# Kernel optimization log

Measured on AMD Instinct MI355X. Metric: run time of the kernel, lower is better.

## Reference

```python
import jax, jax.numpy as jnp
import numpy as np

N_NODES = 50000
N_EDGES = 800000


def setup_inputs() -> dict:
    key = jax.random.key(0)
    ks = jax.random.split(key, 9)
    d, h, hd = 128, 4, 32
    s = 1.0 / np.sqrt(d)
    return {
        "x": jax.random.normal(ks[0], (N_NODES, d), jnp.float32),
        "edge_index": jax.random.randint(ks[1], (2, N_EDGES), 0, N_NODES, jnp.int32),
        "W0": jax.random.normal(ks[2], (d, d), jnp.float32) * s,
        "att_l0": jax.random.normal(ks[3], (h, hd), jnp.float32) * s,
        "att_r0": jax.random.normal(ks[4], (h, hd), jnp.float32) * s,
        "b0": jnp.zeros((d,), jnp.float32),
        "W1": jax.random.normal(ks[5], (d, d), jnp.float32) * s,
        "att_l1": jax.random.normal(ks[6], (h, hd), jnp.float32) * s,
        "att_r1": jax.random.normal(ks[7], (h, hd), jnp.float32) * s,
        "b1": jnp.zeros((hd,), jnp.float32),
    }


def _gat_layer(x, src, dst, W, att_l, att_r, bias, concat):
    # x: [N, F_in]; W: [H*D, F_in] (torch Linear layout); att_*: [H, D]
    n = x.shape[0]
    h, d = att_l.shape
    hx = (x @ W.T).reshape(n, h, d)                     # [N,H,D]
    al = jnp.einsum('nhd,hd->nh', hx, att_l)            # [N,H]
    ar = jnp.einsum('nhd,hd->nh', hx, att_r)
    att = al[src] + ar[dst]                             # [E,H]
    att = jax.nn.leaky_relu(att, negative_slope=0.2)
    # segment softmax over destination nodes
    m = jax.ops.segment_max(att, dst, num_segments=n)   # [N,H]
    att = jnp.exp(att - m[dst])
    ssum = jax.ops.segment_sum(att, dst, num_segments=n)
    att = att / (ssum[dst] + 1e-9)                      # [E,H]
    msgs = att[:, :, None] * hx[src]                    # [E,H,D]
    out = jax.ops.segment_sum(msgs, dst, num_segments=n)  # [N,H,D]
    if concat:
        out = out.reshape(n, h * d)
    else:
        out = out.mean(axis=1)
    return out + bias


def reference(x, edge_index, W0, att_l0, att_r0, b0, W1, att_l1, att_r1, b1):
    src, dst = edge_index[0], edge_index[1]
    x = _gat_layer(x, src, dst, W0, att_l0, att_r0, b0, concat=True)
    x = jax.nn.relu(x)  # dropout is identity in eval mode
    x = _gat_layer(x, src, dst, W1, att_l1, att_r1, b1, concat=False)
    return x
```

## Files before the change

kernel.cpp:

```cpp
#include <hip/hip_runtime.h>
#include <hip/hip_bf16.h>

#define H 4
#define D 32
#define F 128
#define MAXDEG 64
#define PF 16
#define NBUCK 256
#define BUCKW 196
#define NABLK 128
#define SEGCAP 64
#define GB    1563
#define HXP   136

typedef __attribute__((ext_vector_type(8))) short bf16x8;
typedef __attribute__((ext_vector_type(4))) float f32x4;

__device__ __forceinline__ short f2bf(float v) {
    __hip_bfloat16 h = __float2bfloat16(v);
    return *reinterpret_cast<short*>(&h);
}
__device__ __forceinline__ float bf2f(short s) {
    __hip_bfloat16 h = *reinterpret_cast<__hip_bfloat16*>(&s);
    return __bfloat162float(h);
}

__device__ __forceinline__
void wconv_part(int part8, const float* __restrict__ W0, short* __restrict__ W0hi,
                short* __restrict__ W0lo, const float* __restrict__ W1,
                short* __restrict__ W1hi, short* __restrict__ W1lo) {
    const int tid = threadIdx.x;
    const float* W  = (part8 < 4) ? W0 : W1;
    short* Whi = (part8 < 4) ? W0hi : W1hi;
    short* Wlo = (part8 < 4) ? W0lo : W1lo;
    const int part = part8 & 3;
    const int base = part * (F * F / 4);
    for (int i = base + tid * 4; i < base + F * F / 4; i += 1024) {
        float4 v = *reinterpret_cast<const float4*>(W + i);
        float vv[4] = {v.x, v.y, v.z, v.w};
        short hs[4], ls[4];
#pragma unroll
        for (int j = 0; j < 4; ++j) {
            hs[j] = f2bf(vv[j]);
            ls[j] = f2bf(vv[j] - bf2f(hs[j]));
        }
        *reinterpret_cast<short4*>(Whi + i) = make_short4(hs[0], hs[1], hs[2], hs[3]);
        *reinterpret_cast<short4*>(Wlo + i) = make_short4(ls[0], ls[1], ls[2], ls[3]);
    }
}

__device__ __forceinline__
void bucketA_body(int abid, const int* __restrict__ ei, int E,
                  int* __restrict__ cntmat, unsigned int* __restrict__ buf) {
    __shared__ int lcnt[NBUCK];
    const int tid = threadIdx.x;
    lcnt[tid] = 0;
    __syncthreads();
    const int per = ((E / NABLK) + 3) & ~3;
    const int e0 = abid * per;
    const int e1 = min(e0 + per, E);
    for (int e = e0 + 4 * tid; e < e1; e += 1024) {
        int4 dv = *reinterpret_cast<const int4*>(ei + E + e);
        atomicAdd(&lcnt[dv.x / BUCKW], 1);
        atomicAdd(&lcnt[dv.y / BUCKW], 1);
        atomicAdd(&lcnt[dv.z / BUCKW], 1);
        atomicAdd(&lcnt[dv.w / BUCKW], 1);
    }
    __syncthreads();
    cntmat[abid * NBUCK + tid] = min(lcnt[tid], SEGCAP);
    lcnt[tid] = 0;
    __syncthreads();
    for (int e = e0 + 4 * tid; e < e1; e += 1024) {
        int4 sv = *reinterpret_cast<const int4*>(ei + e);
        int4 dv = *reinterpret_cast<const int4*>(ei + E + e);
        int ss[4] = {sv.x, sv.y, sv.z, sv.w};
        int dd[4] = {dv.x, dv.y, dv.z, dv.w};
#pragma unroll
        for (int j = 0; j < 4; ++j) {
            int b = dd[j] / BUCKW;
            int pos = atomicAdd(&lcnt[b], 1);
            if (pos < SEGCAP)
                buf[((size_t)b * NABLK + abid) * SEGCAP + pos] =
                    (unsigned)ss[j] | ((unsigned)(dd[j] - b * BUCKW) << 16);
        }
    }
}

__global__ __launch_bounds__(256)
void k_init(const int* __restrict__ ei, int E, int* __restrict__ cntmat,
            unsigned int* __restrict__ buf,
            const float* __restrict__ W0, short* __restrict__ W0hi,
            short* __restrict__ W0lo, const float* __restrict__ W1,
            short* __restrict__ W1hi, short* __restrict__ W1lo) {
    const int bid = blockIdx.x;
    if (bid < NABLK)
        bucketA_body(bid, ei, E, cntmat, buf);
    else
        wconv_part(bid - NABLK, W0, W0hi, W0lo, W1, W1hi, W1lo);
}

__device__ __forceinline__
void bucketB_body(int b, const unsigned int* __restrict__ buf,
                  const int* __restrict__ cntmat, int* __restrict__ deg,
                  unsigned short* __restrict__ ssrc2u, int N,
                  int* cnt, int* scnt, unsigned short* slots) {
    const int tid = threadIdx.x;
    if (tid < BUCKW) cnt[tid] = 0;
    if (tid < NABLK) scnt[tid] = cntmat[tid * NBUCK + b];
    __syncthreads();
    const int a    = tid & (NABLK - 1);
    const int half = tid >> 7;
    const int mm   = scnt[a];
    const unsigned int* seg = buf + ((size_t)b * NABLK + a) * SEGCAP;
    for (int c = half * 4; c < mm; c += 8) {
        uint4 r = *reinterpret_cast<const uint4*>(seg + c);
        unsigned rr[4] = {r.x, r.y, r.z, r.w};
#pragma unroll
        for (int j = 0; j < 4; ++j) {
            if (c + j < mm) {
                int src  = rr[j] & 0xffff;
                int ldst = rr[j] >> 16;
                int slot = atomicAdd(&cnt[ldst], 1);
                if (slot < MAXDEG)
                    slots[ldst * MAXDEG + slot] = (unsigned short)src;
            }
        }
    }
    __syncthreads();
    uint4* dst = reinterpret_cast<uint4*>(ssrc2u + (size_t)b * BUCKW * MAXDEG);
    const uint4* s4 = reinterpret_cast<const uint4*>(slots);
    for (int i = tid; i < BUCKW * MAXDEG / 8; i += 256)
        dst[i] = s4[i];
    if (tid < BUCKW) {
        int node = b * BUCKW + tid;
        if (node < N) deg[node] = cnt[tid];
    }
}

__device__ __forceinline__
void bsetup_pre(const short* __restrict__ Whi, const short* __restrict__ Wlo,
                int wave, int m, int q8, bf16x8 Bhi[2][4], bf16x8 Blo[2][4]) {
#pragma unroll
    for (int j = 0; j < 2; ++j) {
        const int fout = wave * 32 + j * 16 + m;
#pragma unroll
        for (int kc = 0; kc < 4; ++kc) {
            Bhi[j][kc] = *reinterpret_cast<const bf16x8*>(Whi + (size_t)fout * F + kc * 32 + q8);
            Blo[j][kc] = *reinterpret_cast<const bf16x8*>(Wlo + (size_t)fout * F + kc * 32 + q8);
        }
    }
}

__device__ __forceinline__
void loadA_f32(const float* __restrict__ X, int node0, int m, int q8, float4 r[8]) {
    const float* xp = X + (size_t)(node0 + m) * F + q8;
#pragma unroll
    for (int kc = 0; kc < 4; ++kc) {
        r[2 * kc]     = *reinterpret_cast<const float4*>(xp + kc * 32);
        r[2 * kc + 1] = *reinterpret_cast<const float4*>(xp + kc * 32 + 4);
    }
}

__device__ __forceinline__
void splitA(const float4 r[8], bf16x8 Ahi[4], bf16x8 Alo[4]) {
#pragma unroll
    for (int kc = 0; kc < 4; ++kc) {
        float xv[8] = {r[2 * kc].x, r[2 * kc].y, r[2 * kc].z, r[2 * kc].w,
                       r[2 * kc + 1].x, r[2 * kc + 1].y, r[2 * kc + 1].z, r[2 * kc + 1].w};
#pragma unroll
        for (int t2 = 0; t2 < 8; ++t2) {
            short hh = f2bf(xv[t2]);
            Ahi[kc][t2] = hh;
            Alo[kc][t2] = f2bf(xv[t2] - bf2f(hh));
        }
    }
}

__device__ __forceinline__
void loadA_bf(const short* __restrict__ Xhi, const short* __restrict__ Xlo,
              int node0, int m, int q8, bf16x8 Ahi[4], bf16x8 Alo[4]) {
    const short* xh = Xhi + (size_t)(node0 + m) * F + q8;
    const short* xl = Xlo + (size_t)(node0 + m) * F + q8;
#pragma unroll
    for (int kc = 0; kc < 4; ++kc) {
        Ahi[kc] = *reinterpret_cast<const bf16x8*>(xh + kc * 32);
        Alo[kc] = *reinterpret_cast<const bf16x8*>(xl + kc * 32);
    }
}

__device__ __forceinline__
void mfma_epi(int tile, const bf16x8 Ahi[4], const bf16x8 Alo[4],
              const bf16x8 Bhi[2][4], const bf16x8 Blo[2][4],
              float alw0, float alw16, float arw0, float arw16,
              short* hxs, float* __restrict__ AL,
              float* __restrict__ AR, int wave, int m, int q) {
    const int node0 = tile * 16;
    f32x4 acc0 = {0.f, 0.f, 0.f, 0.f};
    f32x4 acc1 = {0.f, 0.f, 0.f, 0.f};
#pragma unroll
    for (int kc = 0; kc < 4; ++kc) {
        acc0 = __builtin_amdgcn_mfma_f32_16x16x32_bf16(Ahi[kc], Bhi[0][kc], acc0, 0, 0, 0);
        acc1 = __builtin_amdgcn_mfma_f32_16x16x32_bf16(Ahi[kc], Bhi[1][kc], acc1, 0, 0, 0);
        acc0 = __builtin_amdgcn_mfma_f32_16x16x32_bf16(Ahi[kc], Blo[0][kc], acc0, 0, 0, 0);
        acc1 = __builtin_amdgcn_mfma_f32_16x16x32_bf16(Ahi[kc], Blo[1][kc], acc1, 0, 0, 0);
        acc0 = __builtin_amdgcn_mfma_f32_16x16x32_bf16(Alo[kc], Bhi[0][kc], acc0, 0, 0, 0);
        acc1 = __builtin_amdgcn_mfma_f32_16x16x32_bf16(Alo[kc], Bhi[1][kc], acc1, 0, 0, 0);
    }
    const int row0 = node0 + q * 4;
    const int col0 = wave * 32 + m;
#pragma unroll
    for (int r = 0; r < 4; ++r) {
        hxs[(q * 4 + r) * HXP + col0]      = f2bf(acc0[r]);
        hxs[(q * 4 + r) * HXP + col0 + 16] = f2bf(acc1[r]);
        float pal = acc0[r] * alw0 + acc1[r] * alw16;
        float par = acc0[r] * arw0 + acc1[r] * arw16;
#pragma unroll
        for (int o = 1; o < 16; o <<= 1) {
            pal += __shfl_xor(pal, o);
            par += __shfl_xor(par, o);
        }
        if (m == 0) {
            AL[(size_t)(row0 + r) * H + wave] = pal;
            AR[(size_t)(row0 + r) * H + wave] = par;
        }
    }
}

__device__ __forceinline__
void hxb_writeout(const short* hxs, int tile, __hip_bfloat16* __restrict__ HXB) {
    const int tid = threadIdx.x;
    const int row = tid >> 4;
    const int col = (tid & 15) * 8;
    uint4 v = *reinterpret_cast<const uint4*>(hxs + row * HXP + col);
    *reinterpret_cast<uint4*>(reinterpret_cast<short*>(HXB) +
                              (size_t)(tile * 16 + row) * F + col) = v;
}

__device__ __forceinline__
void gemm_pair_f32(int bid, const float* __restrict__ X,
                   const short* __restrict__ Whi, const short* __restrict__ Wlo,
                   const float* __restrict__ attl, const float* __restrict__ attr,
                   __hip_bfloat16* __restrict__ HXB, float* __restrict__ AL,
                   float* __restrict__ AR, int ntiles, short* hxs) {
    const int wave = threadIdx.x >> 6;
    const int lane = threadIdx.x & 63;
    const int m    = lane & 15;
    const int q    = lane >> 4;
    const int q8   = q * 8;
    bf16x8 Bhi[2][4], Blo[2][4];
    bsetup_pre(Whi, Wlo, wave, m, q8, Bhi, Blo);
    const float alw0  = attl[wave * 32 + m];
    const float alw16 = attl[wave * 32 + 16 + m];
    const float arw0  = attr[wave * 32 + m];
    const float arw16 = attr[wave * 32 + 16 + m];

    const int t0 = bid, t1 = bid + GB;
    const bool has1 = t1 < ntiles;
    float4 r0[8], r1[8];
    loadA_f32(X, t0 * 16, m, q8, r0);
    if (has1) loadA_f32(X, t1 * 16, m, q8, r1);
    bf16x8 Ahi[4], Alo[4];
    splitA(r0, Ahi, Alo);
    mfma_epi(t0, Ahi, Alo, Bhi, Blo, alw0, alw16, arw0, arw16, hxs, AL, AR, wave, m, q);
    if (has1) {
        splitA(r1, Ahi, Alo);
        mfma_epi(t1, Ahi, Alo, Bhi, Blo, alw0, alw16, arw0, arw16,
                 hxs + 16 * HXP, AL, AR, wave, m, q);
    }
    __syncthreads();
    hxb_writeout(hxs, t0, HXB);
    if (has1) hxb_writeout(hxs + 16 * HXP, t1, HXB);
}

__device__ __forceinline__
void gemm_pair_bf(int bid, const short* __restrict__ Xhi, const short* __restrict__ Xlo,
                  const short* __restrict__ Whi, const short* __restrict__ Wlo,
                  const float* __restrict__ attl, const float* __restrict__ attr,
                  __hip_bfloat16* __restrict__ HXB, float* __restrict__ AL,
                  float* __restrict__ AR, int ntiles, short* hxs) {
    const int wave = threadIdx.x >> 6;
    const int lane = threadIdx.x & 63;
    const int m    = lane & 15;
    const int q    = lane >> 4;
    const int q8   = q * 8;
    bf16x8 Bhi[2][4], Blo[2][4];
    bsetup_pre(Whi, Wlo, wave, m, q8, Bhi, Blo);
    const float alw0  = attl[wave * 32 + m];
    const float alw16 = attl[wave * 32 + 16 + m];
    const float arw0  = attr[wave * 32 + m];
    const float arw16 = attr[wave * 32 + 16 + m];

    const int t0 = bid, t1 = bid + GB;
    const bool has1 = t1 < ntiles;
    bf16x8 A0h[4], A0l[4], A1h[4], A1l[4];
    loadA_bf(Xhi, Xlo, t0 * 16, m, q8, A0h, A0l);
    if (has1) loadA_bf(Xhi, Xlo, t1 * 16, m, q8, A1h, A1l);
    mfma_epi(t0, A0h, A0l, Bhi, Blo, alw0, alw16, arw0, arw16, hxs, AL, AR, wave, m, q);
    if (has1)
        mfma_epi(t1, A1h, A1l, Bhi, Blo, alw0, alw16, arw0, arw16,
                 hxs + 16 * HXP, AL, AR, wave, m, q);
    __syncthreads();
    hxb_writeout(hxs, t0, HXB);
    if (has1) hxb_writeout(hxs + 16 * HXP, t1, HXB);
}

__global__ __launch_bounds__(256)
void k_mid(const unsigned int* __restrict__ buf, const int* __restrict__ cntmat,
           int* __restrict__ deg, unsigned short* __restrict__ ssrc2u, int N,
           const float* __restrict__ X, const short* __restrict__ W0hi,
           const short* __restrict__ W0lo, const float* __restrict__ attl0,
           const float* __restrict__ attr0, __hip_bfloat16* __restrict__ HXB,
           float* __restrict__ AL, float* __restrict__ AR, int ntiles) {
    __shared__ union {
        struct {
            int cnt[BUCKW];
            int scnt[NABLK];
            unsigned short slots[BUCKW * MAXDEG];
        } bb;
        short hxs[2 * 16 * HXP];
    } sm;
    const int bid = blockIdx.x;
    if (bid < NBUCK)
        bucketB_body(bid, buf, cntmat, deg, ssrc2u, N,
                     sm.bb.cnt, sm.bb.scnt, sm.bb.slots);
    else
        gemm_pair_f32(bid - NBUCK, X, W0hi, W0lo, attl0, attr0, HXB, AL, AR,
                      ntiles, sm.hxs);
}

__device__ __forceinline__
int stage_node32(int g2, int lt, int n, const unsigned short* __restrict__ ssrc2u,
                 const int* __restrict__ deg, const float* __restrict__ AL,
                 const float4 ar4, int (*sidx)[MAXDEG], float (*sw)[MAXDEG][H]) {
    const int cnt  = min(deg[n], MAXDEG);
    const int rcnt = (cnt + PF - 1) & ~(PF - 1);
    for (int t2 = lt; t2 < rcnt; t2 += 32) {
        if (t2 < cnt) {
            int s = ssrc2u[(size_t)n * MAXDEG + t2];
            sidx[g2][t2] = s;
            float4 al4 = *reinterpret_cast<const float4*>(AL + (size_t)s * H);
            float a0 = al4.x + ar4.x; a0 = a0 > 0.f ? a0 : 0.2f * a0;
            float a1 = al4.y + ar4.y; a1 = a1 > 0.f ? a1 : 0.2f * a1;
            float a2 = al4.z + ar4.z; a2 = a2 > 0.f ? a2 : 0.2f * a2;
            float a3 = al4.w + ar4.w; a3 = a3 > 0.f ? a3 : 0.2f * a3;
            sw[g2][t2][0] = __expf(a0);
            sw[g2][t2][1] = __expf(a1);
            sw[g2][t2][2] = __expf(a2);
            sw[g2][t2][3] = __expf(a3);
        } else {
            sidx[g2][t2] = 0;
            sw[g2][t2][0] = 0.f; sw[g2][t2][1] = 0.f;
            sw[g2][t2][2] = 0.f; sw[g2][t2][3] = 0.f;
        }
    }
    __builtin_amdgcn_wave_barrier();
    return rcnt;
}

__device__ __forceinline__
void gather32(int g2, int lt, int rcnt, const __hip_bfloat16* __restrict__ HXB,
              const int (*sidx)[MAXDEG], const float (*sw)[MAXDEG][H],
              float& a0, float& a1, float& a2, float& a3, float& wsum) {
    const int h = lt >> 3;
    const unsigned short* hx = reinterpret_cast<const unsigned short*>(HXB);
    for (int base = 0; base < rcnt; base += PF) {
        ushort4 v[PF];
#pragma unroll
        for (int j = 0; j < PF; ++j) {
            int s = sidx[g2][base + j];
            v[j] = *reinterpret_cast<const ushort4*>(hx + (size_t)s * F + 4 * lt);
        }
#pragma unroll
        for (int j = 0; j < PF; ++j) {
            float w = sw[g2][base + j][h];
            a0 += w * bf2f((short)v[j].x);
            a1 += w * bf2f((short)v[j].y);
            a2 += w * bf2f((short)v[j].z);
            a3 += w * bf2f((short)v[j].w);
            wsum += w;
        }
    }
}

__global__ __launch_bounds__(256)
void k_aggr0(const unsigned short* __restrict__ ssrc2u, const int* __restrict__ deg,
             const float* __restrict__ AL, const float* __restrict__ AR,
             const __hip_bfloat16* __restrict__ HXB, const float* __restrict__ bias,
             short* __restrict__ X1hi, short* __restrict__ X1lo, int N) {
    __shared__ int   sidx[8][MAXDEG];
    __shared__ float sw[8][MAXDEG][H];
    const int tid = threadIdx.x;
    const int g2  = tid >> 5;
    const int lt  = tid & 31;
    const int n   = blockIdx.x * 8 + g2;
    const float4 ar4 = *reinterpret_cast<const float4*>(AR + (size_t)n * H);
    int rcnt = stage_node32(g2, lt, n, ssrc2u, deg, AL, ar4, sidx, sw);
    float a0 = 0.f, a1 = 0.f, a2 = 0.f, a3 = 0.f, ws = 0.f;
    gather32(g2, lt, rcnt, HXB, sidx, sw, a0, a1, a2, a3, ws);
    float inv = 1.f / (ws + 1e-9f);
    const float4 b4 = *reinterpret_cast<const float4*>(bias + 4 * lt);
    float o0 = fmaxf(a0 * inv + b4.x, 0.f);
    float o1 = fmaxf(a1 * inv + b4.y, 0.f);
    float o2 = fmaxf(a2 * inv + b4.z, 0.f);
    float o3 = fmaxf(a3 * inv + b4.w, 0.f);
    short h0 = f2bf(o0), h1 = f2bf(o1), h2 = f2bf(o2), h3 = f2bf(o3);
    short l0 = f2bf(o0 - bf2f(h0)), l1 = f2bf(o1 - bf2f(h1));
    short l2 = f2bf(o2 - bf2f(h2)), l3 = f2bf(o3 - bf2f(h3));
    uint2 hw, lw;
    hw.x = (unsigned)(unsigned short)h0 | ((unsigned)(unsigned short)h1 << 16);
    hw.y = (unsigned)(unsigned short)h2 | ((unsigned)(unsigned short)h3 << 16);
    lw.x = (unsigned)(unsigned short)l0 | ((unsigned)(unsigned short)l1 << 16);
    lw.y = (unsigned)(unsigned short)l2 | ((unsigned)(unsigned short)l3 << 16);
    *reinterpret_cast<uint2*>(X1hi + (size_t)n * F + 4 * lt) = hw;
    *reinterpret_cast<uint2*>(X1lo + (size_t)n * F + 4 * lt) = lw;
}

__global__ __launch_bounds__(256)
void k_gemm1(const short* __restrict__ X1hi, const short* __restrict__ X1lo,
             const short* __restrict__ W1hi, const short* __restrict__ W1lo,
             const float* __restrict__ attl, const float* __restrict__ attr,
             __hip_bfloat16* __restrict__ HXB, float* __restrict__ AL,
             float* __restrict__ AR, int ntiles) {
    __shared__ short hxs[2 * 16 * HXP];
    gemm_pair_bf(blockIdx.x, X1hi, X1lo, W1hi, W1lo, attl, attr,
                 HXB, AL, AR, ntiles, hxs);
}

__global__ __launch_bounds__(256)
void k_aggr1(const unsigned short* __restrict__ ssrc2u, const int* __restrict__ deg,
             const float* __restrict__ AL, const float* __restrict__ AR,
             const __hip_bfloat16* __restrict__ HXB, const float* __restrict__ bias,
             float* __restrict__ out, int N) {
    __shared__ int   sidx[8][MAXDEG];
    __shared__ float sw[8][MAXDEG][H];
    const int tid = threadIdx.x;
    const int g2  = tid >> 5;
    const int lt  = tid & 31;
    const int n   = blockIdx.x * 8 + g2;
    const float4 ar4 = *reinterpret_cast<const float4*>(AR + (size_t)n * H);
    int rcnt = stage_node32(g2, lt, n, ssrc2u, deg, AL, ar4, sidx, sw);
    float a0 = 0.f, a1 = 0.f, a2 = 0.f, a3 = 0.f, ws = 0.f;
    gather32(g2, lt, rcnt, HXB, sidx, sw, a0, a1, a2, a3, ws);
    float inv = 1.f / (ws + 1e-9f);
    float v0 = a0 * inv, v1 = a1 * inv, v2 = a2 * inv, v3 = a3 * inv;
    v0 += __shfl_xor(v0, 8);  v1 += __shfl_xor(v1, 8);
    v2 += __shfl_xor(v2, 8);  v3 += __shfl_xor(v3, 8);
    v0 += __shfl_xor(v0, 16); v1 += __shfl_xor(v1, 16);
    v2 += __shfl_xor(v2, 16); v3 += __shfl_xor(v3, 16);
    if (lt < 8) {
        const float4 b4 = *reinterpret_cast<const float4*>(bias + 4 * lt);
        float4 o;
        o.x = 0.25f * v0 + b4.x;
        o.y = 0.25f * v1 + b4.y;
        o.z = 0.25f * v2 + b4.z;
        o.w = 0.25f * v3 + b4.w;
        *reinterpret_cast<float4*>(out + (size_t)n * D + 4 * lt) = o;
    }
}

extern "C" void kernel_launch(void* const* d_in, const int* in_sizes, int n_in,
                              void* d_out, int out_size, void* d_ws, size_t ws_size,
                              hipStream_t stream) {
    const float* x     = (const float*)d_in[0];
    const int*   ei    = (const int*)d_in[1];
    const float* W0    = (const float*)d_in[2];
    const float* attl0 = (const float*)d_in[3];
    const float* attr0 = (const float*)d_in[4];
    const float* b0    = (const float*)d_in[5];
    const float* W1    = (const float*)d_in[6];
    const float* attl1 = (const float*)d_in[7];
    const float* attr1 = (const float*)d_in[8];
    const float* b1    = (const float*)d_in[9];

    const int N = in_sizes[0] / F;
    const int E = in_sizes[1] / 2;
    const int ntiles = N / 16;

    char* p = (char*)d_ws;
    __hip_bfloat16* HXB = (__hip_bfloat16*)p;   p += (size_t)N * F * 2;
    short* X1hi = (short*)p;                    p += (size_t)N * F * 2;
    short* X1lo = (short*)p;                    p += (size_t)N * F * 2;
    short* W0hi = (short*)p;                    p += (size_t)F * F * 2;
    short* W0lo = (short*)p;                    p += (size_t)F * F * 2;
    short* W1hi = (short*)p;                    p += (size_t)F * F * 2;
    short* W1lo = (short*)p;                    p += (size_t)F * F * 2;
    float* AL   = (float*)p;                    p += (size_t)N * H * 4;
    float* AR   = (float*)p;                    p += (size_t)N * H * 4;
    unsigned short* ssrc2u = (unsigned short*)p;
    p += (size_t)NBUCK * BUCKW * MAXDEG * 2;
    int* deg = (int*)p;                         p += (size_t)N * 4;
    unsigned int* buf = (unsigned int*)p;       p += (size_t)NBUCK * NABLK * SEGCAP * 4;
    int* cntmat = (int*)p;

    k_init<<<NABLK + 8, 256, 0, stream>>>(ei, E, cntmat, buf,
                                          W0, W0hi, W0lo, W1, W1hi, W1lo);

    k_mid<<<NBUCK + GB, 256, 0, stream>>>(buf, cntmat, deg, ssrc2u, N,
                                          x, W0hi, W0lo, attl0, attr0,
                                          HXB, AL, AR, ntiles);

    k_aggr0<<<N / 8, 256, 0, stream>>>(ssrc2u, deg, AL, AR, HXB, b0,
                                       X1hi, X1lo, N);

    k_gemm1<<<GB, 256, 0, stream>>>(X1hi, X1lo, W1hi, W1lo, attl1, attr1,
                                    HXB, AL, AR, ntiles);

    k_aggr1<<<N / 8, 256, 0, stream>>>(ssrc2u, deg, AL, AR, HXB, b1,
                                       (float*)d_out, N);
}
```

Before: 222.6 us.

## Fuse layer-0 aggregation with layer-1 GEMM in one kernel via LDS tile

Merges the layer-0 aggregation kernel and the layer-1 projection GEMM into one kernel. Each block aggregates 16 nodes, stores the split hi/lo bf16 activations in shared memory, and then runs the MFMA GEMM on that tile. This removes the X1hi/X1lo global round-trip and one kernel launch. HXB, AL and AR are double-buffered so the fused kernel never overwrites layer-0 data that other blocks are still reading. The cost is one GEMM tile per block instead of two, more LDS use, and possibly lower occupancy.

Result: faster. 214.8 us (-3.5%).

```diff
diff --git a/kernel.cpp b/kernel.cpp
--- a/kernel.cpp
+++ b/kernel.cpp
@@ -173,18 +173,6 @@
             Ahi[kc][t2] = hh;
             Alo[kc][t2] = f2bf(xv[t2] - bf2f(hh));
         }
-    }
-}
-
-__device__ __forceinline__
-void loadA_bf(const short* __restrict__ Xhi, const short* __restrict__ Xlo,
-              int node0, int m, int q8, bf16x8 Ahi[4], bf16x8 Alo[4]) {
-    const short* xh = Xhi + (size_t)(node0 + m) * F + q8;
-    const short* xl = Xlo + (size_t)(node0 + m) * F + q8;
-#pragma unroll
-    for (int kc = 0; kc < 4; ++kc) {
-        Ahi[kc] = *reinterpret_cast<const bf16x8*>(xh + kc * 32);
-        Alo[kc] = *reinterpret_cast<const bf16x8*>(xl + kc * 32);
     }
 }
 
@@ -267,38 +255,6 @@
         mfma_epi(t1, Ahi, Alo, Bhi, Blo, alw0, alw16, arw0, arw16,
                  hxs + 16 * HXP, AL, AR, wave, m, q);
     }
-    __syncthreads();
-    hxb_writeout(hxs, t0, HXB);
-    if (has1) hxb_writeout(hxs + 16 * HXP, t1, HXB);
-}
-
-__device__ __forceinline__
-void gemm_pair_bf(int bid, const short* __restrict__ Xhi, const short* __restrict__ Xlo,
-                  const short* __restrict__ Whi, const short* __restrict__ Wlo,
-                  const float* __restrict__ attl, const float* __restrict__ attr,
-                  __hip_bfloat16* __restrict__ HXB, float* __restrict__ AL,
-                  float* __restrict__ AR, int ntiles, short* hxs) {
-    const int wave = threadIdx.x >> 6;
-    const int lane = threadIdx.x & 63;
-    const int m    = lane & 15;
-    const int q    = lane >> 4;
-    const int q8   = q * 8;
-    bf16x8 Bhi[2][4], Blo[2][4];
-    bsetup_pre(Whi, Wlo, wave, m, q8, Bhi, Blo);
-    const float alw0  = attl[wave * 32 + m];
-    const float alw16 = attl[wave * 32 + 16 + m];
-    const float arw0  = attr[wave * 32 + m];
-    const float arw16 = attr[wave * 32 + 16 + m];
-
-    const int t0 = bid, t1 = bid + GB;
-    const bool has1 = t1 < ntiles;
-    bf16x8 A0h[4], A0l[4], A1h[4], A1l[4];
-    loadA_bf(Xhi, Xlo, t0 * 16, m, q8, A0h, A0l);
-    if (has1) loadA_bf(Xhi, Xlo, t1 * 16, m, q8, A1h, A1l);
-    mfma_epi(t0, A0h, A0l, Bhi, Blo, alw0, alw16, arw0, arw16, hxs, AL, AR, wave, m, q);
-    if (has1)
-        mfma_epi(t1, A1h, A1l, Bhi, Blo, alw0, alw16, arw0, arw16,
-                 hxs + 16 * HXP, AL, AR, wave, m, q);
     __syncthreads();
     hxb_writeout(hxs, t0, HXB);
     if (has1) hxb_writeout(hxs + 16 * HXP, t1, HXB);
@@ -383,47 +339,73 @@
 }
 
 __global__ __launch_bounds__(256)
-void k_aggr0(const unsigned short* __restrict__ ssrc2u, const int* __restrict__ deg,
-             const float* __restrict__ AL, const float* __restrict__ AR,
-             const __hip_bfloat16* __restrict__ HXB, const float* __restrict__ bias,
-             short* __restrict__ X1hi, short* __restrict__ X1lo, int N) {
+void k_ag1(const unsigned short* __restrict__ ssrc2u, const int* __restrict__ deg,
+           const float* __restrict__ AL0, const float* __restrict__ AR0,
+           const __hip_bfloat16* __restrict__ HXB0, const float* __restrict__ b0,
+           const short* __restrict__ W1hi, const short* __restrict__ W1lo,
+           const float* __restrict__ attl1, const float* __restrict__ attr1,
+           __hip_bfloat16* __restrict__ HXB1, float* __restrict__ AL1,
+           float* __restrict__ AR1, int ntiles) {
     __shared__ int   sidx[8][MAXDEG];
     __shared__ float sw[8][MAXDEG][H];
-    const int tid = threadIdx.x;
-    const int g2  = tid >> 5;
-    const int lt  = tid & 31;
-    const int n   = blockIdx.x * 8 + g2;
-    const float4 ar4 = *reinterpret_cast<const float4*>(AR + (size_t)n * H);
-    int rcnt = stage_node32(g2, lt, n, ssrc2u, deg, AL, ar4, sidx, sw);
-    float a0 = 0.f, a1 = 0.f, a2 = 0.f, a3 = 0.f, ws = 0.f;
-    gather32(g2, lt, rcnt, HXB, sidx, sw, a0, a1, a2, a3, ws);
-    float inv = 1.f / (ws + 1e-9f);
-    const float4 b4 = *reinterpret_cast<const float4*>(bias + 4 * lt);
-    float o0 = fmaxf(a0 * inv + b4.x, 0.f);
-    float o1 = fmaxf(a1 * inv + b4.y, 0.f);
-    float o2 = fmaxf(a2 * inv + b4.z, 0.f);
-    float o3 = fmaxf(a3 * inv + b4.w, 0.f);
-    short h0 = f2bf(o0), h1 = f2bf(o1), h2 = f2bf(o2), h3 = f2bf(o3);
-    short l0 = f2bf(o0 - bf2f(h0)), l1 = f2bf(o1 - bf2f(h1));
-    short l2 = f2bf(o2 - bf2f(h2)), l3 = f2bf(o3 - bf2f(h3));
-    uint2 hw, lw;
-    hw.x = (unsigned)(unsigned short)h0 | ((unsigned)(unsigned short)h1 << 16);
-    hw.y = (unsigned)(unsigned short)h2 | ((unsigned)(unsigned short)h3 << 16);
-    lw.x = (unsigned)(unsigned short)l0 | ((unsigned)(unsigned short)l1 << 16);
-    lw.y = (unsigned)(unsigned short)l2 | ((unsigned)(unsigned short)l3 << 16);
-    *reinterpret_cast<uint2*>(X1hi + (size_t)n * F + 4 * lt) = hw;
-    *reinterpret_cast<uint2*>(X1lo + (size_t)n * F + 4 * lt) = lw;
-}
-
-__global__ __launch_bounds__(256)
-void k_gemm1(const short* __restrict__ X1hi, const short* __restrict__ X1lo,
-             const short* __restrict__ W1hi, const short* __restrict__ W1lo,
-             const float* __restrict__ attl, const float* __restrict__ attr,
-             __hip_bfloat16* __restrict__ HXB, float* __restrict__ AL,
-             float* __restrict__ AR, int ntiles) {
-    __shared__ short hxs[2 * 16 * HXP];
-    gemm_pair_bf(blockIdx.x, X1hi, X1lo, W1hi, W1lo, attl, attr,
-                 HXB, AL, AR, ntiles, hxs);
+    __shared__ short x1h[16 * HXP];
+    __shared__ short x1l[16 * HXP];
+    const int tid  = threadIdx.x;
+    const int g2   = tid >> 5;
+    const int lt   = tid & 31;
+    const int tile = blockIdx.x;
+
+#pragma unroll
+    for (int r = 0; r < 2; ++r) {
+        const int n = tile * 16 + r * 8 + g2;
+        const float4 ar4 = *reinterpret_cast<const float4*>(AR0 + (size_t)n * H);
+        int rcnt = stage_node32(g2, lt, n, ssrc2u, deg, AL0, ar4, sidx, sw);
+        float a0 = 0.f, a1 = 0.f, a2 = 0.f, a3 = 0.f, ws = 0.f;
+        gather32(g2, lt, rcnt, HXB0, sidx, sw, a0, a1, a2, a3, ws);
+        float inv = 1.f / (ws + 1e-9f);
+        const float4 b4 = *reinterpret_cast<const float4*>(b0 + 4 * lt);
+        float o0 = fmaxf(a0 * inv + b4.x, 0.f);
+        float o1 = fmaxf(a1 * inv + b4.y, 0.f);
+        float o2 = fmaxf(a2 * inv + b4.z, 0.f);
+        float o3 = fmaxf(a3 * inv + b4.w, 0.f);
+        short h0 = f2bf(o0), h1 = f2bf(o1), h2 = f2bf(o2), h3 = f2bf(o3);
+        short l0 = f2bf(o0 - bf2f(h0)), l1 = f2bf(o1 - bf2f(h1));
+        short l2 = f2bf(o2 - bf2f(h2)), l3 = f2bf(o3 - bf2f(h3));
+        const int row = r * 8 + g2;
+        uint2 hw, lw;
+        hw.x = (unsigned)(unsigned short)h0 | ((unsigned)(unsigned short)h1 << 16);
+        hw.y = (unsigned)(unsigned short)h2 | ((unsigned)(unsigned short)h3 << 16);
+        lw.x = (unsigned)(unsigned short)l0 | ((unsigned)(unsigned short)l1 << 16);
+        lw.y = (unsigned)(unsigned short)l2 | ((unsigned)(unsigned short)l3 << 16);
+        *reinterpret_cast<uint2*>(x1h + row * HXP + 4 * lt) = hw;
+        *reinterpret_cast<uint2*>(x1l + row * HXP + 4 * lt) = lw;
+    }
+    __syncthreads();
+
+    short* hxs = reinterpret_cast<short*>(sw);
+    {
+        const int wave = tid >> 6;
+        const int lane = tid & 63;
+        const int m    = lane & 15;
+        const int q    = lane >> 4;
+        const int q8   = q * 8;
+        bf16x8 Bhi[2][4], Blo[2][4];
+        bsetup_pre(W1hi, W1lo, wave, m, q8, Bhi, Blo);
+        const float alw0  = attl1[wave * 32 + m];
+        const float alw16 = attl1[wave * 32 + 16 + m];
+        const float arw0  = attr1[wave * 32 + m];
+        const float arw16 = attr1[wave * 32 + 16 + m];
+        bf16x8 Ahi[4], Alo[4];
+#pragma unroll
+        for (int kc = 0; kc < 4; ++kc) {
+            Ahi[kc] = *reinterpret_cast<const bf16x8*>(x1h + m * HXP + kc * 32 + q8);
+            Alo[kc] = *reinterpret_cast<const bf16x8*>(x1l + m * HXP + kc * 32 + q8);
+        }
+        mfma_epi(tile, Ahi, Alo, Bhi, Blo, alw0, alw16, arw0, arw16,
+                 hxs, AL1, AR1, wave, m, q);
+    }
+    __syncthreads();
+    hxb_writeout(hxs, tile, HXB1);
 }
 
 __global__ __launch_bounds__(256)
@@ -477,19 +459,20 @@
     const int ntiles = N / 16;
 
     char* p = (char*)d_ws;
-    __hip_bfloat16* HXB = (__hip_bfloat16*)p;   p += (size_t)N * F * 2;
-    short* X1hi = (short*)p;                    p += (size_t)N * F * 2;
-    short* X1lo = (short*)p;                    p += (size_t)N * F * 2;
-    short* W0hi = (short*)p;                    p += (size_t)F * F * 2;
-    short* W0lo = (short*)p;                    p += (size_t)F * F * 2;
-    short* W1hi = (short*)p;                    p += (size_t)F * F * 2;
-    short* W1lo = (short*)p;                    p += (size_t)F * F * 2;
-    float* AL   = (float*)p;                    p += (size_t)N * H * 4;
-    float* AR   = (float*)p;                    p += (size_t)N * H * 4;
+    __hip_bfloat16* HXB0 = (__hip_bfloat16*)p; p += (size_t)N * F * 2;
+    __hip_bfloat16* HXB1 = (__hip_bfloat16*)p; p += (size_t)N * F * 2;
+    short* W0hi = (short*)p;                   p += (size_t)F * F * 2;
+    short* W0lo = (short*)p;                   p += (size_t)F * F * 2;
+    short* W1hi = (short*)p;                   p += (size_t)F * F * 2;
+    short* W1lo = (short*)p;                   p += (size_t)F * F * 2;
+    float* AL0  = (float*)p;                   p += (size_t)N * H * 4;
+    float* AR0  = (float*)p;                   p += (size_t)N * H * 4;
+    float* AL1  = (float*)p;                   p += (size_t)N * H * 4;
+    float* AR1  = (float*)p;                   p += (size_t)N * H * 4;
     unsigned short* ssrc2u = (unsigned short*)p;
     p += (size_t)NBUCK * BUCKW * MAXDEG * 2;
-    int* deg = (int*)p;                         p += (size_t)N * 4;
-    unsigned int* buf = (unsigned int*)p;       p += (size_t)NBUCK * NABLK * SEGCAP * 4;
+    int* deg = (int*)p;                        p += (size_t)N * 4;
+    unsigned int* buf = (unsigned int*)p;      p += (size_t)NBUCK * NABLK * SEGCAP * 4;
     int* cntmat = (int*)p;
 
     k_init<<<NABLK + 8, 256, 0, stream>>>(ei, E, cntmat, buf,
@@ -497,14 +480,12 @@
 
     k_mid<<<NBUCK + GB, 256, 0, stream>>>(buf, cntmat, deg, ssrc2u, N,
                                           x, W0hi, W0lo, attl0, attr0,
-                                          HXB, AL, AR, ntiles);
-
-    k_aggr0<<<N / 8, 256, 0, stream>>>(ssrc2u, deg, AL, AR, HXB, b0,
-                                       X1hi, X1lo, N);
-
-    k_gemm1<<<GB, 256, 0, stream>>>(X1hi, X1lo, W1hi, W1lo, attl1, attr1,
-                                    HXB, AL, AR, ntiles);
-
-    k_aggr1<<<N / 8, 256, 0, stream>>>(ssrc2u, deg, AL, AR, HXB, b1,
+                                          HXB0, AL0, AR0, ntiles);
+
+    k_ag1<<<ntiles, 256, 0, stream>>>(ssrc2u, deg, AL0, AR0, HXB0, b0,
+                                      W1hi, W1lo, attl1, attr1,
+                                      HXB1, AL1, AR1, ntiles);
+
+    k_aggr1<<<N / 8, 256, 0, stream>>>(ssrc2u, deg, AL1, AR1, HXB1, b1,
                                        (float*)d_out, N);
 }
```
